# Kernel optimization log

Hardware: AMD Instinct MI355X
Metric: run time of the kernel (lower is better)

Reference implementation:

```python
import jax, jax.numpy as jnp
import numpy as np

K = 3       # kernel size
PAD = 1
STRIDE = 1


def conv2d(x, w, b):
    # Plain dense 3x3 conv, NCHW / OIHW, stride 1, padding 1 (matches nn.Conv2d).
    y = jax.lax.conv_general_dilated(
        x, w, (STRIDE, STRIDE), ((PAD, PAD), (PAD, PAD)),
        dimension_numbers=('NCHW', 'OIHW', 'NCHW'))
    return y + b[None, :, None, None]


def setup_inputs() -> dict:
    key = jax.random.key(0)
    ks = jax.random.split(key, 6)
    B, Cin, Cout, H, W = 8, 256, 256, 48, 48
    x = jax.random.normal(ks[0], (B, Cin, H, W), jnp.float32)
    # main deform-conv weight (kaiming-like scale)
    weight = jax.random.normal(ks[1], (Cout, Cin, K, K), jnp.float32) * (2.0 / (Cin * K * K)) ** 0.5
    # offset/mask convs: torch inits these to zero; we use small random values so the
    # irregular bilinear-gather path is actually exercised.
    off_w = jax.random.normal(ks[2], (2 * K * K, Cin, K, K), jnp.float32) * 0.01
    off_b = jax.random.normal(ks[3], (2 * K * K,), jnp.float32) * 0.1
    mask_w = jax.random.normal(ks[4], (K * K, Cin, K, K), jnp.float32) * 0.01
    mask_b = jnp.zeros((K * K,), jnp.float32)
    return dict(x=x, weight=weight, off_w=off_w, off_b=off_b, mask_w=mask_w, mask_b=mask_b)


def _bilinear_sample(img, py, px):
    # img: [C,H,W]; py,px: [K2,Ho,Wo] fractional sample coords (zero padding outside).
    C, H, W = img.shape
    y0 = jnp.floor(py)
    x0 = jnp.floor(px)
    wy = py - y0
    wx = px - x0

    def gather(yi, xi):
        yc = jnp.clip(yi, 0, H - 1).astype(jnp.int32)
        xc = jnp.clip(xi, 0, W - 1).astype(jnp.int32)
        valid = ((yi >= 0) & (yi <= H - 1) & (xi >= 0) & (xi <= W - 1)).astype(img.dtype)
        return img[:, yc, xc] * valid  # [C,K2,Ho,Wo]

    return (gather(y0, x0) * (1 - wy) * (1 - wx)
            + gather(y0, x0 + 1) * (1 - wy) * wx
            + gather(y0 + 1, x0) * wy * (1 - wx)
            + gather(y0 + 1, x0 + 1) * wy * wx)


def _deform_conv2d(x, offset, mask, weight):
    # Modulated deformable conv v2 (torchvision layout: offset = (dy,dx) pairs per tap).
    B, Cin, H, W = x.shape
    Cout = weight.shape[0]
    Ho, Wo = H, W  # stride 1, pad 1, k 3 -> same spatial size
    ky, kx = jnp.meshgrid(jnp.arange(K), jnp.arange(K), indexing='ij')
    ky = ky.reshape(-1).astype(x.dtype)  # [K2]
    kx = kx.reshape(-1).astype(x.dtype)
    hs = jnp.arange(Ho, dtype=x.dtype) * STRIDE - PAD
    ws = jnp.arange(Wo, dtype=x.dtype) * STRIDE - PAD
    off = offset.reshape(B, K * K, 2, Ho, Wo)
    py = off[:, :, 0] + ky[None, :, None, None] + hs[None, None, :, None]  # [B,K2,Ho,Wo]
    px = off[:, :, 1] + kx[None, :, None, None] + ws[None, None, None, :]
    sampled = jax.vmap(_bilinear_sample)(x, py, px)  # [B,Cin,K2,Ho,Wo]
    vals = sampled * mask[:, None]                   # modulation
    return jnp.einsum('bckhw,ock->bohw', vals, weight.reshape(Cout, Cin, K * K))


def reference(x, weight, off_w, off_b, mask_w, mask_b):
    offset = conv2d(x, off_w, off_b)
    mask = jax.nn.sigmoid(conv2d(x, mask_w, mask_b))
    return _deform_conv2d(x, offset, mask, weight)
```

## Files before the change

kernel.cpp:

```cpp
#include <hip/hip_runtime.h>
#include <cstdint>
#include <cmath>

#define DEV __device__ __forceinline__

typedef float v4f __attribute__((ext_vector_type(4)));
typedef short v8s __attribute__((ext_vector_type(8)));
typedef short v4s __attribute__((ext_vector_type(4)));

static constexpr int HW    = 48 * 48;
static constexpr int NPOS  = 8 * HW;

DEV float bf2f(unsigned short u) {
  unsigned int v = ((unsigned int)u) << 16;
  float f; __builtin_memcpy(&f, &v, 4); return f;
}
DEV unsigned short f2bf(float f) {
  unsigned int u; __builtin_memcpy(&u, &f, 4);
  unsigned int r = (u + 0x7fffu + ((u >> 16) & 1u)) >> 16;
  return (unsigned short)r;
}

DEV void gload16(const void* g, void* l) {
  __builtin_amdgcn_global_load_lds(
      (const __attribute__((address_space(1))) unsigned int*)g,
      (__attribute__((address_space(3))) unsigned int*)l, 16, 0, 0);
}

__global__ __launch_bounds__(256) void k_prep(const float* __restrict__ off_w,
                                              const float* __restrict__ mask_w,
                                              const float* __restrict__ weight,
                                              unsigned short* __restrict__ Wc2,
                                              unsigned short* __restrict__ zp,
                                              unsigned short* __restrict__ wG) {
  __shared__ float wrow[2304];
  int bid = blockIdx.x, tid = threadIdx.x;
  int i = bid * 256 + tid;
  if (bid < 288) {
    if (i < 256) zp[i] = 0;
    int o = i / 2304, col = i % 2304;
    int t = col >> 8, c = col & 255;
    float v = 0.f;
    if (o < 18)      v = off_w[(o * 256 + c) * 9 + t];
    else if (o < 27) v = mask_w[((o - 18) * 256 + c) * 9 + t];
    Wc2[i] = f2bf(v);
  } else {
    int co = bid - 288;
    const float* wsrc = weight + (size_t)co * 2304;
    for (int k = tid; k < 2304; k += 256) wrow[k] = wsrc[k];
    __syncthreads();
    unsigned short* dst = wG + (size_t)co * 2304;
    #pragma unroll
    for (int k = 0; k < 9; k++)
      dst[k * 256 + tid] = f2bf(wrow[tid * 9 + k]);
  }
}

__global__ void k_xt(const float* __restrict__ x, unsigned short* __restrict__ xT) {
  __shared__ float tile[64][65];
  int bid = blockIdx.x;
  int ct = bid & 3; int hwt = (bid >> 2) % 36; int b = bid / 144;
  int c0 = ct * 64, hw0 = hwt * 64;
  int tl = threadIdx.x & 63, tr = threadIdx.x >> 6;
  const float* xb = x + (size_t)(b * 256 + c0) * 2304 + hw0;
  #pragma unroll
  for (int r = 0; r < 16; r++) {
    int cr = tr + r * 4;
    tile[cr][tl] = xb[(size_t)cr * 2304 + tl];
  }
  __syncthreads();
  unsigned short* xo = xT + ((size_t)b * 2304 + hw0) * 256 + c0;
  #pragma unroll
  for (int r = 0; r < 16; r++) {
    int hr = tr + r * 4;
    xo[(size_t)hr * 256 + tl] = f2bf(tile[tl][hr]);
  }
}

__global__ __launch_bounds__(256) void k_cg(const unsigned short* __restrict__ Wc2,
                                            const unsigned short* __restrict__ xT,
                                            const unsigned short* __restrict__ zp,
                                            float* __restrict__ parS) {
  __shared__ unsigned short ldsA[32 * 64];
  __shared__ unsigned short ldsB[64 * 64];
  int nt = blockIdx.x, kc = blockIdx.y;
  int n0 = nt * 64;
  int b = n0 / 2304, hw0 = n0 % 2304;
  int tid = threadIdx.x, lane = tid & 63, wid = tid >> 6;
  int r = lane & 15, q = lane >> 4;
  int row0 = tid >> 3;
  int sslot = (tid & 7) ^ (row0 & 7);

  int hwA = hw0 + row0,      hA = hwA / 48, wA = hwA % 48;
  int hwB = hw0 + row0 + 32, hB = hwB / 48, wB = hwB % 48;

  v4f acc0 = (v4f){0.f, 0.f, 0.f, 0.f};
  v4f acc1 = (v4f){0.f, 0.f, 0.f, 0.f};

  #pragma unroll
  for (int tt = 0; tt < 3; tt++) {
    int t = kc * 3 + tt;
    int dy = kc - 1, dx = tt - 1;
    int yA = hA + dy, xA = wA + dx;
    int yB = hB + dy, xB = wB + dx;
    bool vA = ((unsigned)yA < 48u) && ((unsigned)xA < 48u);
    bool vB = ((unsigned)yB < 48u) && ((unsigned)xB < 48u);
    const unsigned short* baseA2 = Wc2 + (size_t)row0 * 2304 + t * 256 + sslot * 8;
    const unsigned short* base0 = vA ? xT + ((size_t)(b * 2304 + yA * 48 + xA) * 256 + sslot * 8)
                                     : zp + sslot * 8;
    const unsigned short* base1 = vB ? xT + ((size_t)(b * 2304 + yB * 48 + xB) * 256 + sslot * 8)
                                     : zp + sslot * 8;
    #pragma unroll
    for (int cq = 0; cq < 4; cq++) {
      int c0s = cq * 64;
      __syncthreads();
      gload16(baseA2 + c0s, ldsA + tid * 8);
      gload16(base0  + c0s, ldsB + tid * 8);
      gload16(base1  + c0s, ldsB + 2048 + tid * 8);
      __syncthreads();
      #pragma unroll
      for (int ki = 0; ki < 2; ki++) {
        int sl = ((ki * 4 + q) ^ (r & 7)) * 8;
        v8s a0 = *(const v8s*)&ldsA[r * 64 + sl];
        v8s a1 = *(const v8s*)&ldsA[(16 + r) * 64 + sl];
        v8s bb = *(const v8s*)&ldsB[(wid * 16 + r) * 64 + sl];
        acc0 = __builtin_amdgcn_mfma_f32_16x16x32_bf16(a0, bb, acc0, 0, 0, 0);
        acc1 = __builtin_amdgcn_mfma_f32_16x16x32_bf16(a1, bb, acc1, 0, 0, 0);
      }
    }
  }

  float* pp = parS + (size_t)kc * 32 * NPOS + n0;
  #pragma unroll
  for (int e = 0; e < 4; e++) {
    pp[(size_t)(q * 4 + e) * NPOS      + wid * 16 + r] = acc0[e];
    pp[(size_t)(16 + q * 4 + e) * NPOS + wid * 16 + r] = acc1[e];
  }
}

__global__ __launch_bounds__(256) void k_fin(const float* __restrict__ parS,
                                             const float* __restrict__ off_b,
                                             const float* __restrict__ mask_b,
                                             float* __restrict__ smp) {
  int k = blockIdx.x / 72;
  int pos = (blockIdx.x % 72) * 256 + threadIdx.x;
  float s0 = 0.f, s1 = 0.f, s2 = 0.f;
  #pragma unroll
  for (int g = 0; g < 3; g++) {
    const float* pg = parS + (size_t)g * 32 * NPOS + pos;
    s0 += pg[(size_t)(2 * k)     * NPOS];
    s1 += pg[(size_t)(2 * k + 1) * NPOS];
    s2 += pg[(size_t)(18 + k)    * NPOS];
  }
  int hw = pos % 2304; int h = hw / 48, w = hw % 48;
  float m = 1.f / (1.f + expf(-(s2 + mask_b[k])));
  float* sp = smp + ((size_t)k * NPOS + pos) * 3;
  sp[0] = s0 + off_b[2 * k]     + (float)(k / 3) + (float)h - 1.f;
  sp[1] = s1 + off_b[2 * k + 1] + (float)(k % 3) + (float)w - 1.f;
  sp[2] = m;
}

__global__ __launch_bounds__(256) void k_gather(const unsigned short* __restrict__ xT,
                                                const float* __restrict__ smp,
                                                unsigned short* __restrict__ val) {
  int raw = blockIdx.x;
  int b = raw & 7;
  int it = raw >> 3;
  int wv = threadIdx.x >> 6, lane = threadIdx.x & 63;
  int task = it * 4 + wv;
  int k = task % 9, hw = task / 9;
  int pos = b * 2304 + hw;
  const float* sp = smp + ((size_t)k * NPOS + pos) * 3;
  float py = sp[0], px = sp[1], m = sp[2];
  float y0f = floorf(py), x0f = floorf(px);
  float wy = py - y0f, wx = px - x0f;
  int y0 = (int)y0f, x0 = (int)x0f;
  bool vy0 = (y0 >= 0) && (y0 <= 47), vy1 = (y0 >= -1) && (y0 <= 46);
  bool vx0 = (x0 >= 0) && (x0 <= 47), vx1 = (x0 >= -1) && (x0 <= 46);
  int yc0 = min(max(y0, 0), 47), yc1 = min(max(y0 + 1, 0), 47);
  int xc0 = min(max(x0, 0), 47), xc1 = min(max(x0 + 1, 0), 47);
  float w00 = (1.f - wy) * (1.f - wx) * m * (float)(vy0 && vx0);
  float w01 = (1.f - wy) * wx         * m * (float)(vy0 && vx1);
  float w10 = wy         * (1.f - wx) * m * (float)(vy1 && vx0);
  float w11 = wy         * wx         * m * (float)(vy1 && vx1);
  const unsigned short* xb = xT + (size_t)b * 2304 * 256;
  int ch = lane * 4;
  v4s c00 = *(const v4s*)&xb[(yc0 * 48 + xc0) * 256 + ch];
  v4s c01 = *(const v4s*)&xb[(yc0 * 48 + xc1) * 256 + ch];
  v4s c10 = *(const v4s*)&xb[(yc1 * 48 + xc0) * 256 + ch];
  v4s c11 = *(const v4s*)&xb[(yc1 * 48 + xc1) * 256 + ch];
  unsigned short o[4];
  #pragma unroll
  for (int i = 0; i < 4; i++) {
    float v = w00 * bf2f((unsigned short)c00[i]) + w01 * bf2f((unsigned short)c01[i])
            + w10 * bf2f((unsigned short)c10[i]) + w11 * bf2f((unsigned short)c11[i]);
    o[i] = f2bf(v);
  }
  *(v4s*)&val[(size_t)pos * 2304 + k * 256 + ch] = *(const v4s*)o;
}

__global__ __launch_bounds__(256) void k_gemm(const unsigned short* __restrict__ wG,
                                              const unsigned short* __restrict__ val,
                                              float* __restrict__ out) {
  __shared__ unsigned short ldsA[128 * 64];
  __shared__ unsigned short ldsB[64 * 64];
  int raw = blockIdx.x;
  int xcd = raw & 7, idx = raw >> 3;
  int mt = idx & 1;
  int nt = xcd * 36 + (idx >> 1);
  int co0 = mt * 128, n0 = nt * 64;
  int tid = threadIdx.x, lane = tid & 63, wid = tid >> 6;
  int wm = wid >> 1, wn = wid & 1;
  int r = lane & 15, q = lane >> 4;
  int srow = tid >> 3;
  int sx = ((tid & 7) ^ (srow & 7)) * 8;

  const unsigned short* Ag = wG  + (size_t)(co0 + srow) * 2304 + sx;
  const unsigned short* Bg = val + (size_t)(n0  + srow) * 2304 + sx;

  v4f acc[4][2];
  #pragma unroll
  for (int i = 0; i < 4; i++)
    #pragma unroll
    for (int j = 0; j < 2; j++) acc[i][j] = (v4f){0.f, 0.f, 0.f, 0.f};

  for (int ks = 0; ks < 36; ks++) {
    int k0 = ks * 64;
    __syncthreads();
    #pragma unroll
    for (int i = 0; i < 4; i++)
      gload16(Ag + k0 + (size_t)i * 32 * 2304, ldsA + i * 2048 + tid * 8);
    #pragma unroll
    for (int i = 0; i < 2; i++)
      gload16(Bg + k0 + (size_t)i * 32 * 2304, ldsB + i * 2048 + tid * 8);
    __syncthreads();
    #pragma unroll
    for (int ki = 0; ki < 2; ki++) {
      int sl = ((ki * 4 + q) ^ (r & 7)) * 8;
      v8s af[4], bf[2];
      #pragma unroll
      for (int fm = 0; fm < 4; fm++)
        af[fm] = *(const v8s*)&ldsA[(wm * 64 + fm * 16 + r) * 64 + sl];
      #pragma unroll
      for (int fn = 0; fn < 2; fn++)
        bf[fn] = *(const v8s*)&ldsB[(wn * 32 + fn * 16 + r) * 64 + sl];
      #pragma unroll
      for (int fm = 0; fm < 4; fm++)
        #pragma unroll
        for (int fn = 0; fn < 2; fn++)
          acc[fm][fn] = __builtin_amdgcn_mfma_f32_16x16x32_bf16(af[fm], bf[fn], acc[fm][fn], 0, 0, 0);
    }
  }

  int bimg = n0 / 2304, hw0 = n0 % 2304;
  float* op = out + (size_t)bimg * (256 * 2304) + hw0;
  #pragma unroll
  for (int fm = 0; fm < 4; fm++) {
    int co = co0 + wm * 64 + fm * 16 + q * 4;
    #pragma unroll
    for (int fn = 0; fn < 2; fn++) {
      int nn = wn * 32 + fn * 16 + r;
      #pragma unroll
      for (int e = 0; e < 4; e++)
        op[(size_t)(co + e) * 2304 + nn] = acc[fm][fn][e];
    }
  }
}

extern "C" void kernel_launch(void* const* d_in, const int* in_sizes, int n_in,
                              void* d_out, int out_size, void* d_ws, size_t ws_size,
                              hipStream_t stream) {
  const float* x      = (const float*)d_in[0];
  const float* weight = (const float*)d_in[1];
  const float* off_w  = (const float*)d_in[2];
  const float* off_b  = (const float*)d_in[3];
  const float* mask_w = (const float*)d_in[4];
  const float* mask_b = (const float*)d_in[5];
  float* out = (float*)d_out;
  char* ws = (char*)d_ws;

  unsigned short* xT   = (unsigned short*)(ws);
  unsigned short* wG   = (unsigned short*)(ws + 9437184);
  unsigned short* Wc2  = (unsigned short*)(ws + 10616832);
  unsigned short* zp   = (unsigned short*)(ws + 10764288);
  float*          smp  = (float*)(ws + 10764800);
  float*          parS = (float*)(ws + 12755456);
  unsigned short* val  = (unsigned short*)(ws + 12755456);

  hipLaunchKernelGGL(k_prep,   dim3(544),      dim3(256), 0, stream,
                     off_w, mask_w, weight, Wc2, zp, wG);
  hipLaunchKernelGGL(k_xt,     dim3(1152),     dim3(256), 0, stream, x, xT);
  hipLaunchKernelGGL(k_cg,     dim3(288, 3),   dim3(256), 0, stream, Wc2, xT, zp, parS);
  hipLaunchKernelGGL(k_fin,    dim3(648),      dim3(256), 0, stream, parS, off_b, mask_b, smp);
  hipLaunchKernelGGL(k_gather, dim3(41472),    dim3(256), 0, stream, xT, smp, val);
  hipLaunchKernelGGL(k_gemm,   dim3(576),      dim3(256), 0, stream, wG, val, out);
}
```

Before: 95.04 us.

## Split-K the offset conv and main GEMM, merge prep and transpose kernels

```diff
diff --git a/kernel.cpp b/kernel.cpp
--- a/kernel.cpp
+++ b/kernel.cpp
@@ -27,16 +27,40 @@
       (__attribute__((address_space(3))) unsigned int*)l, 16, 0, 0);
 }
 
-__global__ __launch_bounds__(256) void k_prep(const float* __restrict__ off_w,
-                                              const float* __restrict__ mask_w,
-                                              const float* __restrict__ weight,
-                                              unsigned short* __restrict__ Wc2,
-                                              unsigned short* __restrict__ zp,
-                                              unsigned short* __restrict__ wG) {
-  __shared__ float wrow[2304];
+__global__ __launch_bounds__(256) void k_pre(const float* __restrict__ x,
+                                             const float* __restrict__ off_w,
+                                             const float* __restrict__ mask_w,
+                                             const float* __restrict__ weight,
+                                             unsigned short* __restrict__ xT,
+                                             unsigned short* __restrict__ Wc2,
+                                             unsigned short* __restrict__ zp,
+                                             unsigned short* __restrict__ wG,
+                                             float* __restrict__ out) {
+  __shared__ float tile[64][65];
   int bid = blockIdx.x, tid = threadIdx.x;
-  int i = bid * 256 + tid;
-  if (bid < 288) {
+  if (bid < 1152) {
+    v4f* o4 = (v4f*)out;
+    #pragma unroll
+    for (int i = 0; i < 4; i++)
+      o4[(size_t)bid * 1024 + i * 256 + tid] = (v4f){0.f, 0.f, 0.f, 0.f};
+    int ct = bid & 3; int hwt = (bid >> 2) % 36; int b = bid / 144;
+    int c0 = ct * 64, hw0 = hwt * 64;
+    int tl = tid & 63, tr = tid >> 6;
+    const float* xb = x + (size_t)(b * 256 + c0) * 2304 + hw0;
+    #pragma unroll
+    for (int r = 0; r < 16; r++) {
+      int cr = tr + r * 4;
+      tile[cr][tl] = xb[(size_t)cr * 2304 + tl];
+    }
+    __syncthreads();
+    unsigned short* xo = xT + ((size_t)b * 2304 + hw0) * 256 + c0;
+    #pragma unroll
+    for (int r = 0; r < 16; r++) {
+      int hr = tr + r * 4;
+      xo[(size_t)hr * 256 + tl] = f2bf(tile[tl][hr]);
+    }
+  } else if (bid < 1440) {
+    int i = (bid - 1152) * 256 + tid;
     if (i < 256) zp[i] = 0;
     int o = i / 2304, col = i % 2304;
     int t = col >> 8, c = col & 255;
@@ -45,35 +69,15 @@
     else if (o < 27) v = mask_w[((o - 18) * 256 + c) * 9 + t];
     Wc2[i] = f2bf(v);
   } else {
-    int co = bid - 288;
+    int co = bid - 1440;
     const float* wsrc = weight + (size_t)co * 2304;
+    float* wrow = &tile[0][0];
     for (int k = tid; k < 2304; k += 256) wrow[k] = wsrc[k];
     __syncthreads();
     unsigned short* dst = wG + (size_t)co * 2304;
     #pragma unroll
     for (int k = 0; k < 9; k++)
       dst[k * 256 + tid] = f2bf(wrow[tid * 9 + k]);
-  }
-}
-
-__global__ void k_xt(const float* __restrict__ x, unsigned short* __restrict__ xT) {
-  __shared__ float tile[64][65];
-  int bid = blockIdx.x;
-  int ct = bid & 3; int hwt = (bid >> 2) % 36; int b = bid / 144;
-  int c0 = ct * 64, hw0 = hwt * 64;
-  int tl = threadIdx.x & 63, tr = threadIdx.x >> 6;
-  const float* xb = x + (size_t)(b * 256 + c0) * 2304 + hw0;
-  #pragma unroll
-  for (int r = 0; r < 16; r++) {
-    int cr = tr + r * 4;
-    tile[cr][tl] = xb[(size_t)cr * 2304 + tl];
-  }
-  __syncthreads();
-  unsigned short* xo = xT + ((size_t)b * 2304 + hw0) * 256 + c0;
-  #pragma unroll
-  for (int r = 0; r < 16; r++) {
-    int hr = tr + r * 4;
-    xo[(size_t)hr * 256 + tl] = f2bf(tile[tl][hr]);
   }
 }
 
@@ -83,7 +87,7 @@
                                             float* __restrict__ parS) {
   __shared__ unsigned short ldsA[32 * 64];
   __shared__ unsigned short ldsB[64 * 64];
-  int nt = blockIdx.x, kc = blockIdx.y;
+  int nt = blockIdx.x, t = blockIdx.y;
   int n0 = nt * 64;
   int b = n0 / 2304, hw0 = n0 % 2304;
   int tid = threadIdx.x, lane = tid & 63, wid = tid >> 6;
@@ -97,40 +101,36 @@
   v4f acc0 = (v4f){0.f, 0.f, 0.f, 0.f};
   v4f acc1 = (v4f){0.f, 0.f, 0.f, 0.f};
 
-  #pragma unroll
-  for (int tt = 0; tt < 3; tt++) {
-    int t = kc * 3 + tt;
-    int dy = kc - 1, dx = tt - 1;
-    int yA = hA + dy, xA = wA + dx;
-    int yB = hB + dy, xB = wB + dx;
-    bool vA = ((unsigned)yA < 48u) && ((unsigned)xA < 48u);
-    bool vB = ((unsigned)yB < 48u) && ((unsigned)xB < 48u);
-    const unsigned short* baseA2 = Wc2 + (size_t)row0 * 2304 + t * 256 + sslot * 8;
-    const unsigned short* base0 = vA ? xT + ((size_t)(b * 2304 + yA * 48 + xA) * 256 + sslot * 8)
-                                     : zp + sslot * 8;
-    const unsigned short* base1 = vB ? xT + ((size_t)(b * 2304 + yB * 48 + xB) * 256 + sslot * 8)
-                                     : zp + sslot * 8;
-    #pragma unroll
-    for (int cq = 0; cq < 4; cq++) {
-      int c0s = cq * 64;
-      __syncthreads();
-      gload16(baseA2 + c0s, ldsA + tid * 8);
-      gload16(base0  + c0s, ldsB + tid * 8);
-      gload16(base1  + c0s, ldsB + 2048 + tid * 8);
-      __syncthreads();
-      #pragma unroll
-      for (int ki = 0; ki < 2; ki++) {
-        int sl = ((ki * 4 + q) ^ (r & 7)) * 8;
-        v8s a0 = *(const v8s*)&ldsA[r * 64 + sl];
-        v8s a1 = *(const v8s*)&ldsA[(16 + r) * 64 + sl];
-        v8s bb = *(const v8s*)&ldsB[(wid * 16 + r) * 64 + sl];
-        acc0 = __builtin_amdgcn_mfma_f32_16x16x32_bf16(a0, bb, acc0, 0, 0, 0);
-        acc1 = __builtin_amdgcn_mfma_f32_16x16x32_bf16(a1, bb, acc1, 0, 0, 0);
-      }
-    }
-  }
-
-  float* pp = parS + (size_t)kc * 32 * NPOS + n0;
+  int dy = t / 3 - 1, dx = t % 3 - 1;
+  int yA = hA + dy, xA = wA + dx;
+  int yB = hB + dy, xB = wB + dx;
+  bool vA = ((unsigned)yA < 48u) && ((unsigned)xA < 48u);
+  bool vB = ((unsigned)yB < 48u) && ((unsigned)xB < 48u);
+  const unsigned short* baseA2 = Wc2 + (size_t)row0 * 2304 + t * 256 + sslot * 8;
+  const unsigned short* base0 = vA ? xT + ((size_t)(b * 2304 + yA * 48 + xA) * 256 + sslot * 8)
+                                   : zp + sslot * 8;
+  const unsigned short* base1 = vB ? xT + ((size_t)(b * 2304 + yB * 48 + xB) * 256 + sslot * 8)
+                                   : zp + sslot * 8;
+  #pragma unroll
+  for (int cq = 0; cq < 4; cq++) {
+    int c0s = cq * 64;
+    __syncthreads();
+    gload16(baseA2 + c0s, ldsA + tid * 8);
+    gload16(base0  + c0s, ldsB + tid * 8);
+    gload16(base1  + c0s, ldsB + 2048 + tid * 8);
+    __syncthreads();
+    #pragma unroll
+    for (int ki = 0; ki < 2; ki++) {
+      int sl = ((ki * 4 + q) ^ (r & 7)) * 8;
+      v8s a0 = *(const v8s*)&ldsA[r * 64 + sl];
+      v8s a1 = *(const v8s*)&ldsA[(16 + r) * 64 + sl];
+      v8s bb = *(const v8s*)&ldsB[(wid * 16 + r) * 64 + sl];
+      acc0 = __builtin_amdgcn_mfma_f32_16x16x32_bf16(a0, bb, acc0, 0, 0, 0);
+      acc1 = __builtin_amdgcn_mfma_f32_16x16x32_bf16(a1, bb, acc1, 0, 0, 0);
+    }
+  }
+
+  float* pp = parS + (size_t)t * 32 * NPOS + n0;
   #pragma unroll
   for (int e = 0; e < 4; e++) {
     pp[(size_t)(q * 4 + e) * NPOS      + wid * 16 + r] = acc0[e];
@@ -146,7 +146,7 @@
   int pos = (blockIdx.x % 72) * 256 + threadIdx.x;
   float s0 = 0.f, s1 = 0.f, s2 = 0.f;
   #pragma unroll
-  for (int g = 0; g < 3; g++) {
+  for (int g = 0; g < 9; g++) {
     const float* pg = parS + (size_t)g * 32 * NPOS + pos;
     s0 += pg[(size_t)(2 * k)     * NPOS];
     s1 += pg[(size_t)(2 * k + 1) * NPOS];
@@ -207,16 +207,18 @@
   int raw = blockIdx.x;
   int xcd = raw & 7, idx = raw >> 3;
   int mt = idx & 1;
-  int nt = xcd * 36 + (idx >> 1);
+  int kc = (idx >> 1) & 1;
+  int nt = xcd * 36 + (idx >> 2);
   int co0 = mt * 128, n0 = nt * 64;
+  int kbase = kc * 1152;
   int tid = threadIdx.x, lane = tid & 63, wid = tid >> 6;
   int wm = wid >> 1, wn = wid & 1;
   int r = lane & 15, q = lane >> 4;
   int srow = tid >> 3;
   int sx = ((tid & 7) ^ (srow & 7)) * 8;
 
-  const unsigned short* Ag = wG  + (size_t)(co0 + srow) * 2304 + sx;
-  const unsigned short* Bg = val + (size_t)(n0  + srow) * 2304 + sx;
+  const unsigned short* Ag = wG  + (size_t)(co0 + srow) * 2304 + kbase + sx;
+  const unsigned short* Bg = val + (size_t)(n0  + srow) * 2304 + kbase + sx;
 
   v4f acc[4][2];
   #pragma unroll
@@ -224,7 +226,7 @@
     #pragma unroll
     for (int j = 0; j < 2; j++) acc[i][j] = (v4f){0.f, 0.f, 0.f, 0.f};
 
-  for (int ks = 0; ks < 36; ks++) {
+  for (int ks = 0; ks < 18; ks++) {
     int k0 = ks * 64;
     __syncthreads();
     #pragma unroll
@@ -262,7 +264,7 @@
       int nn = wn * 32 + fn * 16 + r;
       #pragma unroll
       for (int e = 0; e < 4; e++)
-        op[(size_t)(co + e) * 2304 + nn] = acc[fm][fn][e];
+        unsafeAtomicAdd(&op[(size_t)(co + e) * 2304 + nn], acc[fm][fn][e]);
     }
   }
 }
@@ -287,11 +289,10 @@
   float*          parS = (float*)(ws + 12755456);
   unsigned short* val  = (unsigned short*)(ws + 12755456);
 
-  hipLaunchKernelGGL(k_prep,   dim3(544),      dim3(256), 0, stream,
-                     off_w, mask_w, weight, Wc2, zp, wG);
-  hipLaunchKernelGGL(k_xt,     dim3(1152),     dim3(256), 0, stream, x, xT);
-  hipLaunchKernelGGL(k_cg,     dim3(288, 3),   dim3(256), 0, stream, Wc2, xT, zp, parS);
+  hipLaunchKernelGGL(k_pre,    dim3(1696),     dim3(256), 0, stream,
+                     x, off_w, mask_w, weight, xT, Wc2, zp, wG, out);
+  hipLaunchKernelGGL(k_cg,     dim3(288, 9),   dim3(256), 0, stream, Wc2, xT, zp, parS);
   hipLaunchKernelGGL(k_fin,    dim3(648),      dim3(256), 0, stream, parS, off_b, mask_b, smp);
   hipLaunchKernelGGL(k_gather, dim3(41472),    dim3(256), 0, stream, xT, smp, val);
-  hipLaunchKernelGGL(k_gemm,   dim3(576),      dim3(256), 0, stream, wG, val, out);
-}
+  hipLaunchKernelGGL(k_gemm,   dim3(1152),     dim3(256), 0, stream, wG, val, out);
+}
```

Result: slower. 115.2 us (+21.2%).
